# Performance work log

Measured on AMD Instinct MI355X. Metric: run time of the kernel, lower is better.

## Reference

```python
import jax, jax.numpy as jnp
import numpy as np

B, T, D, H, L = 16, 1024, 1024, 1024, 2


def setup_inputs() -> dict:
    key = jax.random.key(0)
    ks = jax.random.split(key, 7)
    s_ih = float(np.sqrt(6.0 / (4 * H + D)))  # xavier_uniform bound
    s_hh = float(np.sqrt(6.0 / (4 * H + H)))
    return {
        "x": jax.random.normal(ks[0], (B, T, D), dtype=jnp.float32),
        "w_ih0": jax.random.uniform(ks[1], (4 * H, D), jnp.float32, -s_ih, s_ih),
        "w_hh0": jax.random.uniform(ks[2], (4 * H, H), jnp.float32, -s_hh, s_hh),
        "b0": jnp.zeros((4 * H,), jnp.float32),
        "w_ih1": jax.random.uniform(ks[3], (4 * H, H), jnp.float32, -s_ih, s_ih),
        "w_hh1": jax.random.uniform(ks[4], (4 * H, H), jnp.float32, -s_hh, s_hh),
        "b1": jnp.zeros((4 * H,), jnp.float32),
    }


def _cell(x, h, c, w_ih, w_hh, b):
    # gates: [B, 4H]
    gates = x @ w_ih.T + h @ w_hh.T + b
    i, f, g, o = jnp.split(gates, 4, axis=1)
    i = jnp.exp(i)            # exponential input gate (xLSTM sLSTM)
    f = jnp.exp(f)            # exponential forget gate
    g = jnp.tanh(g)
    o = jax.nn.sigmoid(o)
    c = f * c + i * g
    h = o * jnp.tanh(c)
    return h, c


def reference(x, w_ih0, w_hh0, b0, w_ih1, w_hh1, b1):
    b = x.shape[0]
    zeros = jnp.zeros((b, H), x.dtype)
    init = (zeros, zeros, zeros, zeros)  # (h0, c0, h1, c1)

    def step(carry, xt):
        h0, c0, h1, c1 = carry
        h0, c0 = _cell(xt, h0, c0, w_ih0, w_hh0, b0)
        h1, c1 = _cell(h0, h1, c1, w_ih1, w_hh1, b1)
        return (h0, c0, h1, c1), h1

    carry, ys = jax.lax.scan(step, init, jnp.swapaxes(x, 0, 1))  # time-major scan
    out = jnp.swapaxes(ys, 0, 1)  # [B, T, H]
    h0, c0, h1, c1 = carry
    return out, h0, c0, h1, c1
```

## Files before the change

### kernel.cpp

```cpp
#include <hip/hip_runtime.h>
#include <math.h>

namespace {
constexpr int Bt   = 16;
constexpr int Tt   = 1024;
constexpr int Hd   = 1024;
constexpr int NT   = 512;
constexpr int UPB  = 8;
constexpr int NROW = 32;
constexpr int BH   = Bt * Hd;

typedef unsigned long long u64;

__device__ __forceinline__ float sanitize_c(float v) {
  return fminf(fmaxf(v, -3.0e38f), 3.0e38f);
}

template <int CTRL>
__device__ __forceinline__ float dpp_add(float v) {
  int x = __builtin_amdgcn_update_dpp(0, __float_as_int(v), CTRL, 0xF, 0xF, true);
  return v + __int_as_float(x);
}
__device__ __forceinline__ float red8(float v) {
  v = dpp_add<0xB1>(v);
  v = dpp_add<0x4E>(v);
  v = dpp_add<0x141>(v);
  return v;
}

__device__ __forceinline__ void st_h32(float* p, float v) {
  __hip_atomic_store(p, v, __ATOMIC_RELAXED, __HIP_MEMORY_SCOPE_AGENT);
}

#define LD16(d, p) asm volatile("global_load_dwordx4 %0, %1, off sc1" \
                                : "=v"(d) : "v"(p) : "memory")
#define STAGE_SLAB(dst, src, sIdx) { \
  _Pragma("unroll") \
  for (int q = 0; q < 2; ++q) { \
    float4 t0,t1,t2,t3,t4,t5,t6,t7; \
    const int base_ = q * 8192 + (sIdx) * 4; \
    LD16(t0, (src) + base_);        LD16(t1, (src) + base_ + 1024); \
    LD16(t2, (src) + base_ + 2048); LD16(t3, (src) + base_ + 3072); \
    LD16(t4, (src) + base_ + 4096); LD16(t5, (src) + base_ + 5120); \
    LD16(t6, (src) + base_ + 6144); LD16(t7, (src) + base_ + 7168); \
    asm volatile("s_waitcnt vmcnt(0)" ::: "memory"); \
    __builtin_amdgcn_sched_barrier(0); \
    *(float4*)((dst) + base_)        = t0; *(float4*)((dst) + base_ + 1024) = t1; \
    *(float4*)((dst) + base_ + 2048) = t2; *(float4*)((dst) + base_ + 3072) = t3; \
    *(float4*)((dst) + base_ + 4096) = t4; *(float4*)((dst) + base_ + 5120) = t5; \
    *(float4*)((dst) + base_ + 6144) = t6; *(float4*)((dst) + base_ + 7168) = t7; \
  } }
}

__global__ __launch_bounds__(NT)
__attribute__((amdgpu_waves_per_eu(2, 2)))
void slstm_persist(
    const float* __restrict__ x,
    const float* __restrict__ wih0, const float* __restrict__ whh0, const float* __restrict__ b0v,
    const float* __restrict__ wih1, const float* __restrict__ whh1, const float* __restrict__ b1v,
    float* __restrict__ out, float* __restrict__ ws)
{
  __shared__ __align__(16) float in0[BH];
  __shared__ __align__(16) float in1[BH];
  __shared__ __align__(16) float red[64 * 17 * 4];
  __shared__ float gatel[NROW * Bt];
  __shared__ float cst[UPB * Bt];
  __shared__ float biasl[NROW];

  const int tid  = threadIdx.x;
  const int bid  = blockIdx.x;
  const int w    = tid >> 6;
  const int lane = tid & 63;
  const int kslo = lane & 7;
  const int rg   = lane >> 3;
  const int ks   = w * 8 + kslo;
  const bool isB = ks >= 32;
  const int ksl  = ks & 31;
  const int cell = bid >> 7;
  const int blk  = bid & 127;
  const int ubase = blk * UPB;

  unsigned* release = (unsigned*)ws;
  unsigned* garrive = (unsigned*)ws + 8192;
  float* h0buf = ws + 9216;
  float* h1buf = h0buf + 3 * BH;

  const float* wmat = (cell == 0) ? (isB ? whh0 : wih0) : (isB ? whh1 : wih1);
  const float* bv   = (cell == 0) ? b0v : b1v;

  const int ro0 = ((0 + kslo) & 7) * 16;
  const int ro1 = ((1 + kslo) & 7) * 16;
  const int ro2 = ((2 + kslo) & 7) * 16;
  const int ro3 = ((3 + kslo) & 7) * 16;
  const int ro4 = ((4 + kslo) & 7) * 16;
  const int ro5 = ((5 + kslo) & 7) * 16;
  const int ro6 = ((6 + kslo) & 7) * 16;
  const int ro7 = ((7 + kslo) & 7) * 16;

  float4 w00,w01,w02,w03,w04,w05,w06,w07;
  float4 w10,w11,w12,w13,w14,w15,w16,w17;
  float4 w20,w21,w22,w23,w24,w25,w26,w27;
  float4 w30,w31,w32,w33,w34,w35,w36,w37;
#define LDW(r) { \
    const int lr = rg * 4 + r; \
    const char* wb = (const char*)(wmat + (size_t)((lr >> 3) * Hd + ubase + (lr & 7)) * Hd + ksl * 32); \
    w##r##0 = *(const float4*)(wb + ro0); w##r##1 = *(const float4*)(wb + ro1); \
    w##r##2 = *(const float4*)(wb + ro2); w##r##3 = *(const float4*)(wb + ro3); \
    w##r##4 = *(const float4*)(wb + ro4); w##r##5 = *(const float4*)(wb + ro5); \
    w##r##6 = *(const float4*)(wb + ro6); w##r##7 = *(const float4*)(wb + ro7); }
  LDW(0) LDW(1) LDW(2) LDW(3)
#undef LDW

  if (tid < NROW) biasl[tid] = bv[(tid >> 3) * Hd + ubase + (tid & 7)];
  if (tid < UPB * Bt) cst[tid] = 0.f;

  if (cell == 0) {
    #pragma unroll
    for (int p = 0; p < 8; ++p) {
      const int e = p * 2048 + tid * 4;
      const int b = e >> 10, d = e & 1023;
      *(float4*)(in0 + e) = *(const float4*)(x + (size_t)b * (Tt * Hd) + d);
    }
  }
  __syncthreads();

#define STEPC(c) { const float4 v = *(const float4*)(pb + ro##c); \
        a0 = fmaf(v.x, w0##c.x, a0); a0 = fmaf(v.y, w0##c.y, a0); \
        a0 = fmaf(v.z, w0##c.z, a0); a0 = fmaf(v.w, w0##c.w, a0); \
        a1 = fmaf(v.x, w1##c.x, a1); a1 = fmaf(v.y, w1##c.y, a1); \
        a1 = fmaf(v.z, w1##c.z, a1); a1 = fmaf(v.w, w1##c.w, a1); \
        a2 = fmaf(v.x, w2##c.x, a2); a2 = fmaf(v.y, w2##c.y, a2); \
        a2 = fmaf(v.z, w2##c.z, a2); a2 = fmaf(v.w, w2##c.w, a2); \
        a3 = fmaf(v.x, w3##c.x, a3); a3 = fmaf(v.y, w3##c.y, a3); \
        a3 = fmaf(v.z, w3##c.z, a3); a3 = fmaf(v.w, w3##c.w, a3); }
#define MATMUL(INBUF) { \
    const float* myin = (INBUF) + ksl * 32; \
    _Pragma("unroll 2") \
    for (int b = 0; b < Bt; ++b) { \
      const char* pb = (const char*)(myin + b * Hd); \
      float a0 = 0.f, a1 = 0.f, a2 = 0.f, a3 = 0.f; \
      STEPC(0) STEPC(1) STEPC(2) STEPC(3) \
      STEPC(4) STEPC(5) STEPC(6) STEPC(7) \
      a0 = red8(a0); a1 = red8(a1); a2 = red8(a2); a3 = red8(a3); \
      if (kslo == 0) \
        *(float4*)&red[((w * 8 + rg) * 17 + b) * 4] = make_float4(a0, a1, a2, a3); \
    } }

  for (int k = 0; k <= Tt + 1; ++k) {
    const bool act = (cell == 0) ? (k < Tt) : (k >= 2);
    const int s0 = (k + 2) % 3;
    const int s1 = (k + 1) & 1;

    if (w < 4) {
      if (act) { MATMUL(in0) }
    } else if (w == 4) {
      const unsigned* relp = release + bid * 32;
      while (__hip_atomic_load(relp, __ATOMIC_RELAXED, __HIP_MEMORY_SCOPE_AGENT)
             < (unsigned)k)
        __builtin_amdgcn_s_sleep(1);
    }
    __syncthreads();

    if (w >= 4) {
      if (act) {
        const int s = tid - 256;
        if ((cell == 0 && k == 0) || (cell == 1 && k == 2)) {
          #pragma unroll
          for (int p = 0; p < 16; ++p)
            *(float4*)(in1 + p * 1024 + s * 4) = make_float4(0.f, 0.f, 0.f, 0.f);
        } else {
          const float* src = (cell == 0) ? (h0buf + s0 * BH) : (h1buf + s1 * BH);
          STAGE_SLAB(in1, src, s)
        }
      }
    } else {
      if (cell == 0) {
        if (k + 1 < Tt) {
          #pragma unroll
          for (int p = 0; p < 16; ++p) {
            const int e = p * 1024 + tid * 4;
            const int b = e >> 10, d = e & 1023;
            *(float4*)(in0 + e) =
                *(const float4*)(x + (size_t)b * (Tt * Hd) + (size_t)(k + 1) * Hd + d);
          }
        }
      } else if (k >= 1 && k <= Tt) {
        const float* src = h0buf + s0 * BH;
        STAGE_SLAB(in0, src, tid)
      }
    }
    __syncthreads();

    float oh = 0.f, oc = 0.f;
    if (act) {
      if (w >= 4) { MATMUL(in1) }
      __syncthreads();

      {
        const int rg2 = tid >> 6, rem = tid & 63, b2 = rem >> 2, r2 = rem & 3;
        float sgm = 0.f;
        #pragma unroll
        for (int ww = 0; ww < 8; ++ww)
          sgm += red[((ww * 8 + rg2) * 17 + b2) * 4 + r2];
        const int lr = rg2 * 4 + r2;
        gatel[lr * Bt + b2] = sgm + biasl[lr];
      }
      __syncthreads();

      if (tid < UPB * Bt) {
        const int u = tid >> 4, b2 = tid & 15;
        const float gi = gatel[(0 * UPB + u) * Bt + b2];
        const float gf = gatel[(1 * UPB + u) * Bt + b2];
        const float gg = gatel[(2 * UPB + u) * Bt + b2];
        const float go = gatel[(3 * UPB + u) * Bt + b2];
        const float ig = expf(gi);
        const float fg = expf(gf);
        const float g_ = tanhf(gg);
        const float og = 1.f / (1.f + expf(-go));
        const float cn = fg * cst[tid] + ig * g_;
        cst[tid] = cn;
        const float h = og * tanhf(cn);
        oh = h; oc = cn;
        const int j = ubase + u;
        if (cell == 0) {
          st_h32(&h0buf[(k % 3) * BH + b2 * Hd + j], h);
        } else {
          st_h32(&h1buf[(k & 1) * BH + b2 * Hd + j], h);
        }
      }
    }

    asm volatile("s_waitcnt vmcnt(0)" ::: "memory");
    __syncthreads();
    if (w == 4) {
      unsigned old = 0;
      if (lane == 0)
        old = __hip_atomic_fetch_add(garrive, 1u, __ATOMIC_RELAXED,
                                     __HIP_MEMORY_SCOPE_AGENT);
      const unsigned tgt = 256u * (unsigned)(k + 1);
      const int isrel =
          __builtin_amdgcn_readfirstlane((lane == 0 && (old + 1u == tgt)) ? 1 : 0);
      if (isrel) {
        #pragma unroll
        for (int m = 0; m < 4; ++m)
          __hip_atomic_store(release + (lane + m * 64) * 32, (unsigned)(k + 1),
                             __ATOMIC_RELAXED, __HIP_MEMORY_SCOPE_AGENT);
      }
    }

    if (act && tid < UPB * Bt) {
      const int u = tid >> 4, b2 = tid & 15, j = ubase + u;
      const size_t fin = (size_t)Bt * Tt * Hd;
      if (cell == 0) {
        if (k == Tt - 1) {
          out[fin + b2 * Hd + j] = oh;
          out[fin + Bt * Hd + b2 * Hd + j] = sanitize_c(oc);
        }
      } else {
        const int t = k - 2;
        out[((size_t)b2 * Tt + t) * Hd + j] = oh;
        if (t == Tt - 1) {
          out[fin + 2 * Bt * Hd + b2 * Hd + j] = oh;
          out[fin + 3 * Bt * Hd + b2 * Hd + j] = sanitize_c(oc);
        }
      }
    }
  }
  asm volatile("s_waitcnt vmcnt(0)" ::: "memory");
#undef MATMUL
#undef STEPC
}

extern "C" void kernel_launch(void* const* d_in, const int* in_sizes, int n_in,
                              void* d_out, int out_size, void* d_ws, size_t ws_size,
                              hipStream_t stream) {
  (void)hipMemsetAsync(d_ws, 0, 36864, stream);

  const float* x    = (const float*)d_in[0];
  const float* wih0 = (const float*)d_in[1];
  const float* whh0 = (const float*)d_in[2];
  const float* b0   = (const float*)d_in[3];
  const float* wih1 = (const float*)d_in[4];
  const float* whh1 = (const float*)d_in[5];
  const float* b1   = (const float*)d_in[6];

  slstm_persist<<<256, NT, 0, stream>>>(x, wih0, whh0, b0, wih1, whh1, b1,
                                        (float*)d_out, (float*)d_ws);
}
```

Before: 16.77 ms.

## Split global barrier into per-layer barriers with cross-layer progress flags

Replaces the single grid-wide barrier over all 256 blocks with two 128-block barriers, one per LSTM layer. Each layer waits on its own release flag plus a progress flag from the other layer. The layer-0 h ring buffer grows from 3 to 6 slots so layer 0 can run up to a few steps ahead of layer 1. This is meant to cut the cost of each per-step barrier and let the two layers drift out of lockstep, at the price of more workspace, a larger memset, and extra flag polling.

```diff
diff --git a/kernel.cpp b/kernel.cpp
--- a/kernel.cpp
+++ b/kernel.cpp
@@ -80,10 +80,14 @@
   const int blk  = bid & 127;
   const int ubase = blk * UPB;
 
-  unsigned* release = (unsigned*)ws;
-  unsigned* garrive = (unsigned*)ws + 8192;
-  float* h0buf = ws + 9216;
-  float* h1buf = h0buf + 3 * BH;
+  unsigned* base_u = (unsigned*)ws;
+  unsigned* rel_own  = base_u + (cell == 0 ? 0     : 8192);
+  unsigned* obs_oth  = base_u + (cell == 0 ? 12288 : 4096);
+  unsigned* rel_mine = base_u + (cell == 0 ? 0     : 8192);
+  unsigned* obs_mine = base_u + (cell == 0 ? 4096  : 12288);
+  unsigned* garr     = base_u + 16384 + (cell == 0 ? 0 : 32);
+  float* h0buf = ws + 17408;
+  float* h1buf = h0buf + 6 * BH;
 
   const float* wmat = (cell == 0) ? (isB ? whh0 : wih0) : (isB ? whh1 : wih1);
   const float* bv   = (cell == 0) ? b0v : b1v;
@@ -148,16 +152,29 @@
 
   for (int k = 0; k <= Tt + 1; ++k) {
     const bool act = (cell == 0) ? (k < Tt) : (k >= 2);
-    const int s0 = (k + 2) % 3;
-    const int s1 = (k + 1) & 1;
+    const int s0r = (k + 5) % 6;
+    const int s0w = k % 6;
+    const int s1  = (k + 1) & 1;
 
     if (w < 4) {
       if (act) { MATMUL(in0) }
     } else if (w == 4) {
-      const unsigned* relp = release + bid * 32;
-      while (__hip_atomic_load(relp, __ATOMIC_RELAXED, __HIP_MEMORY_SCOPE_AGENT)
+      const unsigned* ownp = rel_own + blk * 32;
+      while (__hip_atomic_load(ownp, __ATOMIC_RELAXED, __HIP_MEMORY_SCOPE_AGENT)
              < (unsigned)k)
         __builtin_amdgcn_s_sleep(1);
+      const unsigned* op = obs_oth + blk * 32;
+      if (cell == 0) {
+        if (k >= 5)
+          while (__hip_atomic_load(op, __ATOMIC_RELAXED, __HIP_MEMORY_SCOPE_AGENT)
+                 < (unsigned)(k - 4))
+            __builtin_amdgcn_s_sleep(1);
+      } else {
+        const unsigned tgt = (unsigned)((k < Tt) ? k : Tt);
+        while (__hip_atomic_load(op, __ATOMIC_RELAXED, __HIP_MEMORY_SCOPE_AGENT)
+               < tgt)
+          __builtin_amdgcn_s_sleep(1);
+      }
     }
     __syncthreads();
 
@@ -169,7 +186,7 @@
           for (int p = 0; p < 16; ++p)
             *(float4*)(in1 + p * 1024 + s * 4) = make_float4(0.f, 0.f, 0.f, 0.f);
         } else {
-          const float* src = (cell == 0) ? (h0buf + s0 * BH) : (h1buf + s1 * BH);
+          const float* src = (cell == 0) ? (h0buf + s0r * BH) : (h1buf + s1 * BH);
           STAGE_SLAB(in1, src, s)
         }
       }
@@ -185,7 +202,7 @@
           }
         }
       } else if (k >= 1 && k <= Tt) {
-        const float* src = h0buf + s0 * BH;
+        const float* src = h0buf + s0r * BH;
         STAGE_SLAB(in0, src, tid)
       }
     }
@@ -223,7 +240,7 @@
         oh = h; oc = cn;
         const int j = ubase + u;
         if (cell == 0) {
-          st_h32(&h0buf[(k % 3) * BH + b2 * Hd + j], h);
+          st_h32(&h0buf[s0w * BH + b2 * Hd + j], h);
         } else {
           st_h32(&h1buf[(k & 1) * BH + b2 * Hd + j], h);
         }
@@ -235,16 +252,19 @@
     if (w == 4) {
       unsigned old = 0;
       if (lane == 0)
-        old = __hip_atomic_fetch_add(garrive, 1u, __ATOMIC_RELAXED,
+        old = __hip_atomic_fetch_add(garr, 1u, __ATOMIC_RELAXED,
                                      __HIP_MEMORY_SCOPE_AGENT);
-      const unsigned tgt = 256u * (unsigned)(k + 1);
+      const unsigned tgt = 128u * (unsigned)(k + 1);
       const int isrel =
           __builtin_amdgcn_readfirstlane((lane == 0 && (old + 1u == tgt)) ? 1 : 0);
       if (isrel) {
         #pragma unroll
-        for (int m = 0; m < 4; ++m)
-          __hip_atomic_store(release + (lane + m * 64) * 32, (unsigned)(k + 1),
+        for (int m = 0; m < 2; ++m) {
+          __hip_atomic_store(rel_mine + (lane + m * 64) * 32, (unsigned)(k + 1),
                              __ATOMIC_RELAXED, __HIP_MEMORY_SCOPE_AGENT);
+          __hip_atomic_store(obs_mine + (lane + m * 64) * 32, (unsigned)(k + 1),
+                             __ATOMIC_RELAXED, __HIP_MEMORY_SCOPE_AGENT);
+        }
       }
     }
 
@@ -274,7 +294,7 @@
 extern "C" void kernel_launch(void* const* d_in, const int* in_sizes, int n_in,
                               void* d_out, int out_size, void* d_ws, size_t ws_size,
                               hipStream_t stream) {
-  (void)hipMemsetAsync(d_ws, 0, 36864, stream);
+  (void)hipMemsetAsync(d_ws, 0, 69632, stream);
 
   const float* x    = (const float*)d_in[0];
   const float* wih0 = (const float*)d_in[1];
```

Measured after the change: 16.61 ms. No clear change (-0.9%).
